# Kernel tuning notes

Hardware: AMD Instinct MI355X
Metric: run time of the kernel (lower is better)

Reference implementation:

```python
import jax, jax.numpy as jnp
import numpy as np

N_EXPERTS = 64
LN_EPS = 1e-5


def _layer_norm(x, gamma, beta, eps=LN_EPS):
    mu = jnp.mean(x, axis=-1, keepdims=True)
    var = jnp.mean(jnp.square(x - mu), axis=-1, keepdims=True)
    return (x - mu) * jax.lax.rsqrt(var + eps) * gamma + beta


def setup_inputs() -> dict:
    key = jax.random.key(0)
    ks = jax.random.split(key, 4)
    B, T, D, Ff = 2, 1024, 512, 2048
    x = jax.random.normal(ks[0], (B, T, D), dtype=jnp.float32)
    hex_weights = jax.random.uniform(ks[1], (B, T, N_EXPERTS), dtype=jnp.float32)
    W_in = jax.random.normal(ks[2], (N_EXPERTS, Ff, D), dtype=jnp.float32) * (D ** -0.5)
    b_in = jnp.zeros((N_EXPERTS, Ff), dtype=jnp.float32)
    W_out = jax.random.normal(ks[3], (N_EXPERTS, D, Ff), dtype=jnp.float32) * (Ff ** -0.5)
    b_out = jnp.zeros((N_EXPERTS, D), dtype=jnp.float32)
    ln_gamma = jnp.ones((D,), dtype=jnp.float32)
    ln_beta = jnp.zeros((D,), dtype=jnp.float32)
    return {"x": x, "hex_weights": hex_weights, "W_in": W_in, "b_in": b_in,
            "W_out": W_out, "b_out": b_out, "ln_gamma": ln_gamma,
            "ln_beta": ln_beta, "top_k": 4}


def reference(x, hex_weights, W_in, b_in, W_out, b_out, ln_gamma, ln_beta, top_k):
    B, T, D = x.shape
    N = B * T
    x_n = _layer_norm(x, ln_gamma, ln_beta)

    # top-k routing; renormalize the selected weights (matches torch topk + sum-norm)
    top_w, top_idx = jax.lax.top_k(hex_weights, top_k)          # (B,T,k)
    top_w = top_w / (jnp.sum(top_w, axis=-1, keepdims=True) + 1e-8)

    x_flat = x_n.reshape(N, D)
    # Scatter the k normalized weights into a dense (N, 64) routing matrix.
    # Non-selected experts get weight 0, so a dense per-expert sweep computes
    # EXACTLY the same combined output as the per-token gather in the original.
    w_full = jnp.zeros((N, N_EXPERTS), dtype=x.dtype)
    w_full = w_full.at[jnp.arange(N)[:, None], top_idx.reshape(N, top_k)].set(
        top_w.reshape(N, top_k))

    def body(acc, e):
        W_in_e, b_in_e, W_out_e, b_out_e, we = e  # we: (N,)
        h = jax.nn.silu(x_flat @ W_in_e.T + b_in_e)            # (N, d_ff)
        acc = acc + we[:, None] * (h @ W_out_e.T + b_out_e)    # (N, D)
        return acc, None

    acc, _ = jax.lax.scan(body, jnp.zeros_like(x_flat),
                          (W_in, b_in, W_out, b_out, w_full.T))
    return acc.reshape(B, T, D)
```

## Files before the change

### kernel.cpp

```cpp
#include <hip/hip_runtime.h>

#define NTOK 2048
#define DD   512
#define FFD  2048
#define NE   64
#define KSEL 4
#define NPAIR (NTOK*KSEL)
#define BM 192
#define BK 32
#define NT 128
#define HROWS (NPAIR + 256)

typedef short s16x8 __attribute__((ext_vector_type(8)));
typedef float f32x4 __attribute__((ext_vector_type(4)));

typedef const __attribute__((address_space(1))) char* gptr_t;
typedef __attribute__((address_space(3))) char* lptr_t;

static __device__ __forceinline__ unsigned short f2bf(float f) {
    unsigned int u = __builtin_bit_cast(unsigned int, f);
    u += 0x7FFFu + ((u >> 16) & 1u);
    return (unsigned short)(u >> 16);
}

static __device__ __forceinline__ s16x8 cvt8(float4 a, float4 b) {
    s16x8 r;
    r[0] = (short)f2bf(a.x); r[1] = (short)f2bf(a.y);
    r[2] = (short)f2bf(a.z); r[3] = (short)f2bf(a.w);
    r[4] = (short)f2bf(b.x); r[5] = (short)f2bf(b.y);
    r[6] = (short)f2bf(b.z); r[7] = (short)f2bf(b.w);
    return r;
}

__global__ __launch_bounds__(256) void k_ln_route(
    const float* __restrict__ x, const float* __restrict__ hw,
    const float* __restrict__ gamma, const float* __restrict__ beta,
    unsigned short* __restrict__ xn_bf, int* __restrict__ counts,
    int* __restrict__ tok_e, float* __restrict__ tok_w)
{
    const int t = blockIdx.x;
    const int tid = threadIdx.x;
    const float* xr = x + (size_t)t * DD;
    float v0 = xr[tid];
    float v1 = xr[tid + 256];
    float s = v0 + v1, s2 = v0*v0 + v1*v1;
    #pragma unroll
    for (int off = 32; off > 0; off >>= 1) {
        s  += __shfl_down(s, off);
        s2 += __shfl_down(s2, off);
    }
    __shared__ float rsum[4], rsum2[4];
    __shared__ float smu, srs;
    const int wid = tid >> 6, lane = tid & 63;
    if (lane == 0) { rsum[wid] = s; rsum2[wid] = s2; }
    __syncthreads();
    if (tid == 0) {
        float a = 0.f, b = 0.f;
        for (int i = 0; i < 4; ++i) { a += rsum[i]; b += rsum2[i]; }
        float mu  = a * (1.f / DD);
        float var = b * (1.f / DD) - mu * mu;
        smu = mu; srs = rsqrtf(var + 1e-5f);
    }
    __syncthreads();
    const float mu = smu, rstd = srs;
    xn_bf[(size_t)t*DD + tid]       = f2bf((v0 - mu) * rstd * gamma[tid]       + beta[tid]);
    xn_bf[(size_t)t*DD + tid + 256] = f2bf((v1 - mu) * rstd * gamma[tid + 256] + beta[tid + 256]);

    if (tid < 64) {
        float v = hw[(size_t)t*NE + tid];
        int   sel[KSEL]; float sw[KSEL];
        #pragma unroll
        for (int j = 0; j < KSEL; ++j) {
            float m = v; int mi = tid;
            #pragma unroll
            for (int off = 32; off > 0; off >>= 1) {
                float ov = __shfl_xor(m, off);
                int   oi = __shfl_xor(mi, off);
                if (ov > m || (ov == m && oi < mi)) { m = ov; mi = oi; }
            }
            if (tid == mi) v = -1e30f;
            sel[j] = mi; sw[j] = m;
        }
        if (tid == 0) {
            float ssum = sw[0] + sw[1] + sw[2] + sw[3];
            float inv = 1.f / (ssum + 1e-8f);
            #pragma unroll
            for (int j = 0; j < KSEL; ++j) {
                tok_e[t*KSEL + j] = sel[j];
                tok_w[t*KSEL + j] = sw[j] * inv;
                atomicAdd(&counts[sel[j]], 1);
            }
        }
    }
}

__global__ void k_scan(const int* __restrict__ counts, int* __restrict__ offs,
                       int* __restrict__ cursor, int* __restrict__ tile_e,
                       int* __restrict__ tile_r, int* __restrict__ ntiles)
{
    __shared__ int sc[NE], stc[NE];
    const int tid = threadIdx.x;
    sc[tid] = counts[tid];
    __syncthreads();
    int off = 0;
    for (int i = 0; i < tid; ++i) off += sc[i];
    offs[tid] = off; cursor[tid] = off;
    if (tid == NE-1) offs[NE] = off + sc[NE-1];
    int tc = (sc[tid] + BM - 1) / BM;
    stc[tid] = tc;
    __syncthreads();
    int toff = 0;
    for (int i = 0; i < tid; ++i) toff += stc[i];
    for (int j = 0; j < tc; ++j) { tile_e[toff + j] = tid; tile_r[toff + j] = off + j*BM; }
    if (tid == NE-1) *ntiles = toff + tc;
}

__global__ __launch_bounds__(256) void k_scatter(
    const int* __restrict__ tok_e, const float* __restrict__ tok_w,
    int* __restrict__ cursor, int* __restrict__ pair_tok,
    float* __restrict__ pair_w, int* __restrict__ inv)
{
    int i = blockIdx.x * 256 + threadIdx.x;
    if (i >= NPAIR) return;
    int t = i >> 2;
    int e = tok_e[i];
    int slot = atomicAdd(&cursor[e], 1);
    pair_tok[slot] = t;
    pair_w[slot] = tok_w[i];
    inv[i] = slot;
}

template<int KD, bool IS_IN, int NYG>
__global__ __launch_bounds__(256, 4) void k_moe_gemm(
    const unsigned short* __restrict__ Abf,
    const float* __restrict__ W, const float* __restrict__ bias,
    const int* __restrict__ tile_e, const int* __restrict__ tile_r,
    const int* __restrict__ ntiles, const int* __restrict__ offs,
    const int* __restrict__ pr_tok, const float* __restrict__ pr_w,
    unsigned short* __restrict__ Hout, float* __restrict__ Pout)
{
    constexpr int NK = KD / BK;
    const int ti = blockIdx.x / NYG;
    if (ti >= *ntiles) return;
    const int e    = tile_e[ti];
    const int row0 = tile_r[ti];
    const int rend = offs[e + 1];
    const int n0   = (blockIdx.x % NYG) * 64;
    const int NOUT = IS_IN ? FFD : DD;

    __shared__ __align__(16) unsigned short As[2 * BM * BK];
    __shared__ __align__(16) unsigned short Bs[2 * 64 * BK];

    const int tid  = threadIdx.x;
    const int lane = tid & 63, wave = tid >> 6;
    const int lr = lane & 15, lk = lane >> 4;

    const char* asrc[3];
    #pragma unroll
    for (int i = 0; i < 3; ++i) {
        int seg  = wave * 3 + i;
        int r    = seg * 16 + (lane >> 2);
        int cg   = (lane & 3) ^ ((lane >> 2) & 3);
        int grow = row0 + r;
        size_t rowbase;
        if (IS_IN) {
            int tok = (grow < rend) ? pr_tok[grow] : pr_tok[row0];
            rowbase = (size_t)tok * (KD * 2);
        } else {
            rowbase = (size_t)grow * (KD * 2);
        }
        asrc[i] = (const char*)Abf + rowbase + (size_t)cg * 16;
    }

    const float* wsrc0 = W + (size_t)e * NOUT * KD + (size_t)(n0 + (tid >> 2)) * KD + (tid & 3) * 8;
    const int bn = tid >> 2;
    const int bb = ((tid & 3) << 4) ^ ((bn & 3) << 4);

    f32x4 acc[3][4];
    #pragma unroll
    for (int m = 0; m < 3; ++m)
        #pragma unroll
        for (int n = 0; n < 4; ++n)
            acc[m][n] = (f32x4){0.f, 0.f, 0.f, 0.f};

    {
        #pragma unroll
        for (int i = 0; i < 3; ++i)
            __builtin_amdgcn_global_load_lds((gptr_t)asrc[i],
                (lptr_t)((char*)As + (wave * 3 + i) * 1024), 16, 0, 0);
        float4 b0 = *(const float4*)(wsrc0);
        float4 b1 = *(const float4*)(wsrc0 + 4);
        *(s16x8*)((char*)Bs + bn * 64 + bb) = cvt8(b0, b1);
    }
    __syncthreads();

    int buf = 0;
    for (int kt = 0; kt < NK; ++kt) {
        float4 bN0, bN1;
        if (kt + 1 < NK) {
            #pragma unroll
            for (int i = 0; i < 3; ++i)
                __builtin_amdgcn_global_load_lds((gptr_t)(asrc[i] + (size_t)(kt + 1) * (BK * 2)),
                    (lptr_t)((char*)As + (buf ^ 1) * (BM * BK * 2) + (wave * 3 + i) * 1024),
                    16, 0, 0);
            bN0 = *(const float4*)(wsrc0 + (size_t)(kt + 1) * BK);
            bN1 = *(const float4*)(wsrc0 + (size_t)(kt + 1) * BK + 4);
        }
        __builtin_amdgcn_sched_barrier(0);

        {
            const char* Ab = (const char*)As + buf * (BM * BK * 2);
            const char* Bb = (const char*)Bs + buf * (64 * BK * 2);
            const int sw = ((lk ^ (lr & 3)) << 4);
            s16x8 af[3], bfr[4];
            #pragma unroll
            for (int m = 0; m < 3; ++m)
                af[m] = *(const s16x8*)(Ab + (wave * 48 + m * 16 + lr) * 64 + sw);
            #pragma unroll
            for (int n = 0; n < 4; ++n)
                bfr[n] = *(const s16x8*)(Bb + (n * 16 + lr) * 64 + sw);
            #pragma unroll
            for (int m = 0; m < 3; ++m)
                #pragma unroll
                for (int n = 0; n < 4; ++n)
                    acc[m][n] = __builtin_amdgcn_mfma_f32_16x16x32_bf16(af[m], bfr[n], acc[m][n], 0, 0, 0);
        }
        __builtin_amdgcn_sched_barrier(0);

        if (kt + 1 < NK)
            *(s16x8*)((char*)Bs + (buf ^ 1) * (64 * BK * 2) + bn * 64 + bb) = cvt8(bN0, bN1);
        __syncthreads();
        buf ^= 1;
    }

    #pragma unroll
    for (int m = 0; m < 3; ++m) {
        #pragma unroll
        for (int r = 0; r < 4; ++r) {
            int row = row0 + wave * 48 + m * 16 + lk * 4 + r;
            if (row < rend) {
                if (IS_IN) {
                    #pragma unroll
                    for (int n = 0; n < 4; ++n) {
                        int f = n0 + n * 16 + lr;
                        float v = acc[m][n][r] + bias[e * FFD + f];
                        v = v / (1.f + __expf(-v));
                        Hout[(size_t)row * FFD + f] = f2bf(v);
                    }
                } else {
                    float pw = pr_w[row];
                    #pragma unroll
                    for (int n = 0; n < 4; ++n) {
                        int d = n0 + n * 16 + lr;
                        Pout[(size_t)row * DD + d] = (acc[m][n][r] + bias[e * DD + d]) * pw;
                    }
                }
            }
        }
    }
}

__global__ __launch_bounds__(128) void k_combine(
    const float* __restrict__ pout, const int* __restrict__ inv,
    float* __restrict__ out)
{
    const int t = blockIdx.x;
    const int tid = threadIdx.x;
    const float4* p0 = (const float4*)(pout + (size_t)inv[t*4+0]*DD);
    const float4* p1 = (const float4*)(pout + (size_t)inv[t*4+1]*DD);
    const float4* p2 = (const float4*)(pout + (size_t)inv[t*4+2]*DD);
    const float4* p3 = (const float4*)(pout + (size_t)inv[t*4+3]*DD);
    float4 a = p0[tid], b = p1[tid], c = p2[tid], d = p3[tid];
    float4 r;
    r.x = a.x + b.x + c.x + d.x;
    r.y = a.y + b.y + c.y + d.y;
    r.z = a.z + b.z + c.z + d.z;
    r.w = a.w + b.w + c.w + d.w;
    ((float4*)(out + (size_t)t*DD))[tid] = r;
}

extern "C" void kernel_launch(void* const* d_in, const int* in_sizes, int n_in,
                              void* d_out, int out_size, void* d_ws, size_t ws_size,
                              hipStream_t stream)
{
    const float* x     = (const float*)d_in[0];
    const float* hw    = (const float*)d_in[1];
    const float* Win   = (const float*)d_in[2];
    const float* bin   = (const float*)d_in[3];
    const float* Wout  = (const float*)d_in[4];
    const float* bout  = (const float*)d_in[5];
    const float* gamma = (const float*)d_in[6];
    const float* beta  = (const float*)d_in[7];
    float* out = (float*)d_out;

    char* ws = (char*)d_ws;
    size_t o = 0;
    unsigned short* xn_bf = (unsigned short*)(ws + o); o += (size_t)NTOK * DD * 2;
    unsigned short* H     = (unsigned short*)(ws + o); o += (size_t)HROWS * FFD * 2;
    float* pout   = (float*)(ws + o); o += (size_t)NPAIR * DD * 4;
    int*   counts = (int*)(ws + o);   o += 256;
    int*   offs   = (int*)(ws + o);   o += 512;
    int*   cursor = (int*)(ws + o);   o += 256;
    int*   tok_e  = (int*)(ws + o);   o += (size_t)NPAIR * 4;
    float* tok_w  = (float*)(ws + o); o += (size_t)NPAIR * 4;
    int*   inv    = (int*)(ws + o);   o += (size_t)NPAIR * 4;
    int*   pr_tok = (int*)(ws + o);   o += (size_t)NPAIR * 4;
    float* pr_w   = (float*)(ws + o); o += (size_t)NPAIR * 4;
    int*   tile_e = (int*)(ws + o);   o += 512;
    int*   tile_r = (int*)(ws + o);   o += 512;
    int*   ntiles = (int*)(ws + o);   o += 256;
    (void)ws_size; (void)in_sizes; (void)n_in; (void)out_size;

    hipMemsetAsync(counts, 0, 256, stream);
    k_ln_route<<<dim3(NTOK), dim3(256), 0, stream>>>(x, hw, gamma, beta, xn_bf, counts, tok_e, tok_w);
    k_scan<<<dim3(1), dim3(64), 0, stream>>>(counts, offs, cursor, tile_e, tile_r, ntiles);
    k_scatter<<<dim3(NPAIR/256), dim3(256), 0, stream>>>(tok_e, tok_w, cursor, pr_tok, pr_w, inv);

    k_moe_gemm<DD, true, FFD/64><<<dim3(NT * (FFD/64)), dim3(256), 0, stream>>>(
        xn_bf, Win, bin, tile_e, tile_r, ntiles, offs, pr_tok, pr_w, H, nullptr);
    k_moe_gemm<FFD, false, DD/64><<<dim3(NT * (DD/64)), dim3(256), 0, stream>>>(
        H, Wout, bout, tile_e, tile_r, ntiles, offs, pr_tok, pr_w, nullptr, pout);

    k_combine<<<dim3(NTOK), dim3(128), 0, stream>>>(pout, inv, out);
}
```

Measured before the change: 265.8 us.

## Retile MoE GEMM to 96-row, 128-deep tiles with a 2x2 wave grid

Shrinks the MoE GEMM row tile from 192 to 96 and deepens the K tile from 32 to 128. The four waves are rearranged into a 2x2 grid over M and N, with a new 16-chunk XOR swizzle in shared memory. Weight loads become nontemporal 32-float chunks per thread, and the grid grows to allow up to 192 tiles. The aim is less padding waste per expert and fewer K-loop synchronisations. The trade-off is that experts now span more row tiles, so the fp32 weights may be streamed more than once, and nontemporal hints may stop those repeat reads from hitting in cache.

```diff
diff --git a/kernel.cpp b/kernel.cpp
--- a/kernel.cpp
+++ b/kernel.cpp
@@ -6,13 +6,14 @@
 #define NE   64
 #define KSEL 4
 #define NPAIR (NTOK*KSEL)
-#define BM 192
-#define BK 32
-#define NT 128
+#define BM 96
+#define BK 128
+#define NT2 192
 #define HROWS (NPAIR + 256)
 
 typedef short s16x8 __attribute__((ext_vector_type(8)));
 typedef float f32x4 __attribute__((ext_vector_type(4)));
+typedef float vf4 __attribute__((ext_vector_type(4)));
 
 typedef const __attribute__((address_space(1))) char* gptr_t;
 typedef __attribute__((address_space(3))) char* lptr_t;
@@ -23,7 +24,7 @@
     return (unsigned short)(u >> 16);
 }
 
-static __device__ __forceinline__ s16x8 cvt8(float4 a, float4 b) {
+static __device__ __forceinline__ s16x8 cvt8(vf4 a, vf4 b) {
     s16x8 r;
     r[0] = (short)f2bf(a.x); r[1] = (short)f2bf(a.y);
     r[2] = (short)f2bf(a.z); r[3] = (short)f2bf(a.w);
@@ -131,7 +132,7 @@
 }
 
 template<int KD, bool IS_IN, int NYG>
-__global__ __launch_bounds__(256, 4) void k_moe_gemm(
+__global__ __launch_bounds__(256, 2) void k_moe_gemm(
     const unsigned short* __restrict__ Abf,
     const float* __restrict__ W, const float* __restrict__ bias,
     const int* __restrict__ tile_e, const int* __restrict__ tile_r,
@@ -154,13 +155,15 @@
     const int tid  = threadIdx.x;
     const int lane = tid & 63, wave = tid >> 6;
     const int lr = lane & 15, lk = lane >> 4;
-
-    const char* asrc[3];
+    const int wmbase = (wave & 1) * 48;
+    const int wnbase = (wave >> 1) * 32;
+
+    const char* asrc[6];
     #pragma unroll
-    for (int i = 0; i < 3; ++i) {
-        int seg  = wave * 3 + i;
-        int r    = seg * 16 + (lane >> 2);
-        int cg   = (lane & 3) ^ ((lane >> 2) & 3);
+    for (int i = 0; i < 6; ++i) {
+        int seg  = wave * 6 + i;
+        int r    = seg * 4 + (lane >> 4);
+        int cg   = (lane & 15) ^ (r & 15);
         int grow = row0 + r;
         size_t rowbase;
         if (IS_IN) {
@@ -172,77 +175,98 @@
         asrc[i] = (const char*)Abf + rowbase + (size_t)cg * 16;
     }
 
-    const float* wsrc0 = W + (size_t)e * NOUT * KD + (size_t)(n0 + (tid >> 2)) * KD + (tid & 3) * 8;
+    const float* wsrc0 = W + (size_t)e * NOUT * KD + (size_t)(n0 + (tid >> 2)) * KD + (tid & 3) * 32;
     const int bn = tid >> 2;
-    const int bb = ((tid & 3) << 4) ^ ((bn & 3) << 4);
-
-    f32x4 acc[3][4];
+    const int bc = (tid & 3) * 4;
+
+    f32x4 acc[3][2];
     #pragma unroll
-    for (int m = 0; m < 3; ++m)
-        #pragma unroll
-        for (int n = 0; n < 4; ++n)
-            acc[m][n] = (f32x4){0.f, 0.f, 0.f, 0.f};
+    for (int m = 0; m < 3; ++m) {
+        acc[m][0] = (f32x4){0.f, 0.f, 0.f, 0.f};
+        acc[m][1] = (f32x4){0.f, 0.f, 0.f, 0.f};
+    }
+
+#define BWRITE(DST, BR)                                                           \
+    _Pragma("unroll")                                                             \
+    for (int j = 0; j < 4; ++j) {                                                 \
+        int c = bc + j;                                                           \
+        *(s16x8*)((char*)(DST) + bn * 256 + ((c ^ (bn & 15)) << 4)) =             \
+            cvt8(BR[2*j], BR[2*j+1]);                                             \
+    }
 
     {
         #pragma unroll
-        for (int i = 0; i < 3; ++i)
+        for (int i = 0; i < 6; ++i)
             __builtin_amdgcn_global_load_lds((gptr_t)asrc[i],
-                (lptr_t)((char*)As + (wave * 3 + i) * 1024), 16, 0, 0);
-        float4 b0 = *(const float4*)(wsrc0);
-        float4 b1 = *(const float4*)(wsrc0 + 4);
-        *(s16x8*)((char*)Bs + bn * 64 + bb) = cvt8(b0, b1);
+                (lptr_t)((char*)As + (wave * 6 + i) * 1024), 16, 0, 0);
+        vf4 breg[8];
+        #pragma unroll
+        for (int j = 0; j < 8; ++j)
+            breg[j] = __builtin_nontemporal_load((const vf4*)(wsrc0 + j * 4));
+        BWRITE((char*)Bs, breg);
     }
     __syncthreads();
 
     int buf = 0;
     for (int kt = 0; kt < NK; ++kt) {
-        float4 bN0, bN1;
+        vf4 bregN[8];
         if (kt + 1 < NK) {
             #pragma unroll
-            for (int i = 0; i < 3; ++i)
+            for (int i = 0; i < 6; ++i)
                 __builtin_amdgcn_global_load_lds((gptr_t)(asrc[i] + (size_t)(kt + 1) * (BK * 2)),
-                    (lptr_t)((char*)As + (buf ^ 1) * (BM * BK * 2) + (wave * 3 + i) * 1024),
+                    (lptr_t)((char*)As + (buf ^ 1) * (BM * BK * 2) + (wave * 6 + i) * 1024),
                     16, 0, 0);
-            bN0 = *(const float4*)(wsrc0 + (size_t)(kt + 1) * BK);
-            bN1 = *(const float4*)(wsrc0 + (size_t)(kt + 1) * BK + 4);
+            #pragma unroll
+            for (int j = 0; j < 8; ++j)
+                bregN[j] = __builtin_nontemporal_load(
+                    (const vf4*)(wsrc0 + (size_t)(kt + 1) * BK + j * 4));
         }
         __builtin_amdgcn_sched_barrier(0);
 
         {
             const char* Ab = (const char*)As + buf * (BM * BK * 2);
             const char* Bb = (const char*)Bs + buf * (64 * BK * 2);
-            const int sw = ((lk ^ (lr & 3)) << 4);
-            s16x8 af[3], bfr[4];
-            #pragma unroll
-            for (int m = 0; m < 3; ++m)
-                af[m] = *(const s16x8*)(Ab + (wave * 48 + m * 16 + lr) * 64 + sw);
-            #pragma unroll
-            for (int n = 0; n < 4; ++n)
-                bfr[n] = *(const s16x8*)(Bb + (n * 16 + lr) * 64 + sw);
-            #pragma unroll
-            for (int m = 0; m < 3; ++m)
+            #pragma unroll
+            for (int h = 0; h < 4; ++h) {
+                s16x8 af[3], bfr[2];
                 #pragma unroll
-                for (int n = 0; n < 4; ++n)
-                    acc[m][n] = __builtin_amdgcn_mfma_f32_16x16x32_bf16(af[m], bfr[n], acc[m][n], 0, 0, 0);
+                for (int m = 0; m < 3; ++m) {
+                    int row = wmbase + m * 16 + lr;
+                    af[m] = *(const s16x8*)(Ab + row * 256 + ((((h << 2) | lk) ^ (row & 15)) << 4));
+                }
+                #pragma unroll
+                for (int n = 0; n < 2; ++n) {
+                    int row = wnbase + n * 16 + lr;
+                    bfr[n] = *(const s16x8*)(Bb + row * 256 + ((((h << 2) | lk) ^ (row & 15)) << 4));
+                }
+                #pragma unroll
+                for (int m = 0; m < 3; ++m) {
+                    acc[m][0] = __builtin_amdgcn_mfma_f32_16x16x32_bf16(af[m], bfr[0], acc[m][0], 0, 0, 0);
+                    acc[m][1] = __builtin_amdgcn_mfma_f32_16x16x32_bf16(af[m], bfr[1], acc[m][1], 0, 0, 0);
+                }
+            }
         }
         __builtin_amdgcn_sched_barrier(0);
 
-        if (kt + 1 < NK)
-            *(s16x8*)((char*)Bs + (buf ^ 1) * (64 * BK * 2) + bn * 64 + bb) = cvt8(bN0, bN1);
+        if (kt + 1 < NK) {
+            char* Bw = (char*)Bs + (buf ^ 1) * (64 * BK * 2);
+            BWRITE(Bw, bregN);
+        }
         __syncthreads();
         buf ^= 1;
     }
+#undef BWRITE
 
     #pragma unroll
     for (int m = 0; m < 3; ++m) {
         #pragma unroll
         for (int r = 0; r < 4; ++r) {
-            int row = row0 + wave * 48 + m * 16 + lk * 4 + r;
+            int row = row0 + wmbase + m * 16 + lk * 4 + r;
             if (row < rend) {
                 if (IS_IN) {
                     #pragma unroll
-                    for (int n = 0; n < 4; ++n) {
-                        int f = n0 + n * 16 + lr;
+                    for (int n = 0; n < 2; ++n) {
+                        int f = n0 + wnbase + n * 16 + lr;
                         float v = acc[m][n][r] + bias[e * FFD + f];
                         v = v / (1.f + __expf(-v));
                         Hout[(size_t)row * FFD + f] = f2bf(v);
@@ -250,8 +274,8 @@
                 } else {
                     float pw = pr_w[row];
                     #pragma unroll
-                    for (int n = 0; n < 4; ++n) {
-                        int d = n0 + n * 16 + lr;
+                    for (int n = 0; n < 2; ++n) {
+                        int d = n0 + wnbase + n * 16 + lr;
                         Pout[(size_t)row * DD + d] = (acc[m][n][r] + bias[e * DD + d]) * pw;
                     }
                 }
@@ -306,8 +330,8 @@
     int*   inv    = (int*)(ws + o);   o += (size_t)NPAIR * 4;
     int*   pr_tok = (int*)(ws + o);   o += (size_t)NPAIR * 4;
     float* pr_w   = (float*)(ws + o); o += (size_t)NPAIR * 4;
-    int*   tile_e = (int*)(ws + o);   o += 512;
-    int*   tile_r = (int*)(ws + o);   o += 512;
+    int*   tile_e = (int*)(ws + o);   o += 1024;
+    int*   tile_r = (int*)(ws + o);   o += 1024;
     int*   ntiles = (int*)(ws + o);   o += 256;
     (void)ws_size; (void)in_sizes; (void)n_in; (void)out_size;
 
@@ -316,9 +340,9 @@
     k_scan<<<dim3(1), dim3(64), 0, stream>>>(counts, offs, cursor, tile_e, tile_r, ntiles);
     k_scatter<<<dim3(NPAIR/256), dim3(256), 0, stream>>>(tok_e, tok_w, cursor, pr_tok, pr_w, inv);
 
-    k_moe_gemm<DD, true, FFD/64><<<dim3(NT * (FFD/64)), dim3(256), 0, stream>>>(
+    k_moe_gemm<DD, true, FFD/64><<<dim3(NT2 * (FFD/64)), dim3(256), 0, stream>>>(
         xn_bf, Win, bin, tile_e, tile_r, ntiles, offs, pr_tok, pr_w, H, nullptr);
-    k_moe_gemm<FFD, false, DD/64><<<dim3(NT * (DD/64)), dim3(256), 0, stream>>>(
+    k_moe_gemm<FFD, false, DD/64><<<dim3(NT2 * (DD/64)), dim3(256), 0, stream>>>(
         H, Wout, bout, tile_e, tile_r, ntiles, offs, pr_tok, pr_w, nullptr, pout);
 
     k_combine<<<dim3(NTOK), dim3(128), 0, stream>>>(pout, inv, out);
```

Result: slower. 617.8 us (+132.4%).
